# Kernel tuning notes

Hardware: AMD Instinct MI355X
Metric: run time of the kernel (lower is better)

Reference implementation:

```python
import jax, jax.numpy as jnp
import numpy as np

N = 100000
E = 1600000
F_IN = 256
HEADS = 8
C1 = 8
NCLS = 16
NEG_SLOPE = 0.2


def setup_inputs() -> dict:
    key = jax.random.key(0)
    ks = jax.random.split(key, 8)
    x = jax.random.normal(ks[0], (N, F_IN), dtype=jnp.float32)
    edge_index = jax.random.randint(ks[1], (2, E), 0, N, dtype=jnp.int64)
    W1 = jax.random.normal(ks[2], (F_IN, HEADS * C1), dtype=jnp.float32) * (1.0 / np.sqrt(F_IN))
    a1_src = jax.random.normal(ks[3], (HEADS, C1), dtype=jnp.float32) * 0.1
    a1_dst = jax.random.normal(ks[4], (HEADS, C1), dtype=jnp.float32) * 0.1
    b1 = jnp.zeros((HEADS * C1,), dtype=jnp.float32)
    W2 = jax.random.normal(ks[5], (HEADS * C1, NCLS), dtype=jnp.float32) * (1.0 / np.sqrt(HEADS * C1))
    a2_src = jax.random.normal(ks[6], (1, NCLS), dtype=jnp.float32) * 0.1
    a2_dst = jax.random.normal(ks[7], (1, NCLS), dtype=jnp.float32) * 0.1
    b2 = jnp.zeros((NCLS,), dtype=jnp.float32)
    return {"x": x, "edge_index": edge_index, "W1": W1, "a1_src": a1_src,
            "a1_dst": a1_dst, "b1": b1, "W2": W2, "a2_src": a2_src,
            "a2_dst": a2_dst, "b2": b2}


def gat_layer(x, src, dst, W, a_src, a_dst, b, heads, out_c, concat):
    n = x.shape[0]
    h = (x @ W).reshape(n, heads, out_c)            # [N,H,C]
    al_src = (h * a_src).sum(-1)                    # [N,H]
    al_dst = (h * a_dst).sum(-1)                    # [N,H]
    e = jax.nn.leaky_relu(al_src[src] + al_dst[dst], NEG_SLOPE)  # [E',H]
    m = jax.ops.segment_max(e, dst, num_segments=n)              # per-dst max
    alpha = jnp.exp(e - m[dst])
    denom = jax.ops.segment_sum(alpha, dst, num_segments=n)
    alpha = alpha / denom[dst]
    out = jax.ops.segment_sum(h[src] * alpha[:, :, None], dst, num_segments=n)  # [N,H,C]
    out = out.reshape(n, heads * out_c) if concat else out.mean(axis=1)
    return out + b


def reference(x, edge_index, W1, a1_src, a1_dst, b1, W2, a2_src, a2_dst, b2):
    # add self-loops (PyG GATConv default)
    loop = jnp.arange(N, dtype=edge_index.dtype)
    src = jnp.concatenate([edge_index[0], loop])
    dst = jnp.concatenate([edge_index[1], loop])
    # dropout layers are identity in eval mode
    h = jax.nn.elu(gat_layer(x, src, dst, W1, a1_src, a1_dst, b1, HEADS, C1, True))
    out = gat_layer(h, src, dst, W2, a2_src, a2_dst, b2, 1, NCLS, False)
    return jax.nn.log_softmax(out, axis=-1)
```

## Files before the change

kernel.cpp:

```cpp
#include <hip/hip_runtime.h>
#include <math.h>

#define NN   100000
#define EE   1600000
#define FIN  256
#define NCLS 16
#define NEG  0.2f

#define NEDGE (EE + NN)
#define WBKT  256
#define NBKT  ((NN + WBKT - 1) / WBKT)
#define CAP   5120
#define ABLK  4096
#define NABLK ((NEDGE + ABLK - 1) / ABLK)

#define OFF_GCNT  0
#define OFF_BASE  392
#define OFF_ROW   784
#define OFF_BKT   100788
#define OFF_ADJ   (OFF_BKT + NBKT*CAP)
#define OFF_H1B   (OFF_ADJ + NEDGE)
#define OFF_H1E   (OFF_H1B + NN*32)
#define OFF_AL1S  (OFF_H1E + NN*32)
#define OFF_AL1D  (OFF_AL1S + NN*8)
#define OFF_H2B   (OFF_AL1D + NN*8)
#define OFF_AL2S  (OFF_H2B + NN*8)
#define OFF_AL2D  (OFF_AL2S + NN)

__device__ __forceinline__ float lrelu(float x) { return x >= 0.f ? x : NEG * x; }
__device__ __forceinline__ unsigned short f2bf(float x) {
    unsigned u = __float_as_uint(x);
    return (unsigned short)((u + 0x7FFF + ((u >> 16) & 1)) >> 16);
}
__device__ __forceinline__ float bf2f(unsigned short b) {
    return __uint_as_float(((unsigned)b) << 16);
}
__device__ __forceinline__ float bflo(unsigned u) { return __uint_as_float(u << 16); }
__device__ __forceinline__ float bfhi(unsigned u) { return __uint_as_float(u & 0xFFFF0000u); }

__global__ __launch_bounds__(256) void k_binA(
    const int* __restrict__ esrc, const int* __restrict__ edst,
    int* __restrict__ gcnt, unsigned* __restrict__ bkt)
{
    __shared__ int lcnt[NBKT];
    __shared__ int lbase[NBKT];
    const int t = threadIdx.x;
    const int e0 = blockIdx.x * ABLK;
    for (int i = t; i < NBKT; i += 256) lcnt[i] = 0;
    __syncthreads();

    unsigned wrd[16];
    unsigned short bb[16], ll[16];
    #pragma unroll
    for (int j = 0; j < 16; ++j) {
        int ei = e0 + j * 256 + t;
        bb[j] = 0xFFFFu;
        if (ei < NEDGE) {
            int s, d;
            if (ei < EE) { s = esrc[ei]; d = edst[ei]; } else { s = d = ei - EE; }
            int b = d >> 8;
            wrd[j] = ((unsigned)s << 8) | (unsigned)(d & 255);
            bb[j] = (unsigned short)b;
            ll[j] = (unsigned short)atomicAdd(&lcnt[b], 1);
        }
    }
    __syncthreads();
    for (int i = t; i < NBKT; i += 256)
        lbase[i] = lcnt[i] ? atomicAdd(&gcnt[i], lcnt[i]) : 0;
    __syncthreads();
    #pragma unroll
    for (int j = 0; j < 16; ++j) {
        if (bb[j] != 0xFFFFu) {
            int b = bb[j];
            bkt[(size_t)b * CAP + lbase[b] + ll[j]] = wrd[j];
        }
    }
}

__global__ __launch_bounds__(512) void k_scanB(
    const int* __restrict__ gcnt, int* __restrict__ base, int* __restrict__ row)
{
    __shared__ int s[512];
    int t = threadIdx.x;
    int v = (t < NBKT) ? gcnt[t] : 0;
    s[t] = v;
    __syncthreads();
    for (int off = 1; off < 512; off <<= 1) {
        int u = (t >= off) ? s[t - off] : 0;
        __syncthreads();
        s[t] += u;
        __syncthreads();
    }
    if (t <= NBKT) base[t] = s[t] - v;
    if (t == 0) row[NN] = NEDGE;
}

__global__ __launch_bounds__(256) void k_binC(
    const int* __restrict__ gcnt, const int* __restrict__ base,
    const unsigned* __restrict__ bkt, int* __restrict__ row, int* __restrict__ adj)
{
    __shared__ unsigned wd[CAP];
    __shared__ int hist[256], pref[256], cnt2[256];
    const int g = blockIdx.x, t = threadIdx.x;
    const int cn = gcnt[g], bs = base[g];
    hist[t] = 0; cnt2[t] = 0;
    __syncthreads();
    for (int i = t; i < cn; i += 256) {
        unsigned w = bkt[(size_t)g * CAP + i];
        wd[i] = w;
        atomicAdd(&hist[w & 255], 1);
    }
    __syncthreads();
    int v = hist[t];
    pref[t] = v;
    __syncthreads();
    for (int off = 1; off < 256; off <<= 1) {
        int u = (t >= off) ? pref[t - off] : 0;
        __syncthreads();
        pref[t] += u;
        __syncthreads();
    }
    int ex = pref[t] - v;
    int n = g * 256 + t;
    if (n < NN) row[n] = bs + ex;
    pref[t] = ex;
    __syncthreads();
    for (int i = t; i < cn; i += 256) {
        unsigned w = wd[i];
        int dl = w & 255;
        int p = atomicAdd(&cnt2[dl], 1);
        adj[bs + pref[dl] + p] = (int)(w >> 8);
    }
}

__global__ __launch_bounds__(256) void k_gemm1(
    const float* __restrict__ x, const float* __restrict__ W1,
    const float* __restrict__ a1s, const float* __restrict__ a1d,
    unsigned short* __restrict__ h1b, float* __restrict__ al1s, float* __restrict__ al1d)
{
    __shared__ float sxT[32][68];
    __shared__ float sW[32][64];
    const int t = threadIdx.x;
    const int n0 = blockIdx.x * 64;
    const int tr = t >> 4, tc = t & 15;

    float acc[4][4] = {};

    for (int kc = 0; kc < 256; kc += 32) {
        __syncthreads();
        #pragma unroll
        for (int it = 0; it < 2; ++it) {
            int i = t + it * 256;
            int r = i >> 3, fj = i & 7;
            int n = n0 + r;
            float4 v = (n < NN) ? *(const float4*)(x + (size_t)n * FIN + kc + fj * 4)
                                : make_float4(0.f, 0.f, 0.f, 0.f);
            sxT[fj * 4 + 0][r] = v.x;
            sxT[fj * 4 + 1][r] = v.y;
            sxT[fj * 4 + 2][r] = v.z;
            sxT[fj * 4 + 3][r] = v.w;
        }
        #pragma unroll
        for (int it = 0; it < 2; ++it) {
            int i = t + it * 256;
            int r = i >> 4, fj = i & 15;
            *(float4*)&sW[r][fj * 4] = *(const float4*)(W1 + (size_t)(kc + r) * 64 + fj * 4);
        }
        __syncthreads();
        #pragma unroll
        for (int k = 0; k < 32; ++k) {
            float4 a = *(const float4*)&sxT[k][tr * 4];
            float4 b = *(const float4*)&sW[k][tc * 4];
            acc[0][0] += a.x * b.x; acc[0][1] += a.x * b.y; acc[0][2] += a.x * b.z; acc[0][3] += a.x * b.w;
            acc[1][0] += a.y * b.x; acc[1][1] += a.y * b.y; acc[1][2] += a.y * b.z; acc[1][3] += a.y * b.w;
            acc[2][0] += a.z * b.x; acc[2][1] += a.z * b.y; acc[2][2] += a.z * b.z; acc[2][3] += a.z * b.w;
            acc[3][0] += a.w * b.x; acc[3][1] += a.w * b.y; acc[3][2] += a.w * b.z; acc[3][3] += a.w * b.w;
        }
    }

    #pragma unroll
    for (int j = 0; j < 4; ++j) {
        int n = n0 + tr * 4 + j;
        if (n < NN) {
            ushort4 v = make_ushort4(f2bf(acc[j][0]), f2bf(acc[j][1]), f2bf(acc[j][2]), f2bf(acc[j][3]));
            *(ushort4*)(h1b + (size_t)n * 64 + tc * 4) = v;
        }
    }

    float sa[4], da[4];
    #pragma unroll
    for (int u = 0; u < 4; ++u) { sa[u] = a1s[tc * 4 + u]; da[u] = a1d[tc * 4 + u]; }
    #pragma unroll
    for (int j = 0; j < 4; ++j) {
        float vs = acc[j][0] * sa[0] + acc[j][1] * sa[1] + acc[j][2] * sa[2] + acc[j][3] * sa[3];
        float vd = acc[j][0] * da[0] + acc[j][1] * da[1] + acc[j][2] * da[2] + acc[j][3] * da[3];
        vs += __shfl_xor(vs, 1, 64);
        vd += __shfl_xor(vd, 1, 64);
        int n = n0 + tr * 4 + j;
        if (!(tc & 1) && n < NN) {
            al1s[n * 8 + (tc >> 1)] = vs;
            al1d[n * 8 + (tc >> 1)] = vd;
        }
    }
}

__global__ __launch_bounds__(256) void k_agg1(
    const int* __restrict__ row, const int* __restrict__ adj,
    const float* __restrict__ al1s, const float* __restrict__ al1d,
    const unsigned* __restrict__ h1b2, const float* __restrict__ b1,
    unsigned* __restrict__ h1e2)
{
    const int wv = threadIdx.x >> 6, lane = threadIdx.x & 63;
    const int n = blockIdx.x * 4 + wv;
    const int q = lane >> 4;
    const int r = lane & 15;
    const int h = r >> 1;
    const float ald = al1d[n * 8 + h];
    const int r0 = row[n], r1 = row[n + 1];

    float dsum = 0.f, ax = 0.f, ay = 0.f, bx = 0.f, by = 0.f;
    for (int c0 = r0; c0 < r1; c0 += 64) {
        int li = c0 + lane;
        int adjv = adj[li < r1 ? li : r0];
        int m = r1 - c0; if (m > 64) m = 64;
        int k = 0;
        for (; k + 16 <= m; k += 16) {
            int s0 = __shfl(adjv, k + 0  + q, 64);
            int s1 = __shfl(adjv, k + 4  + q, 64);
            int s2 = __shfl(adjv, k + 8  + q, 64);
            int s3 = __shfl(adjv, k + 12 + q, 64);
            float a0 = al1s[s0 * 8 + h];
            float a1 = al1s[s1 * 8 + h];
            float a2 = al1s[s2 * 8 + h];
            float a3 = al1s[s3 * 8 + h];
            uint2 u0 = *(const uint2*)(h1b2 + s0 * 32 + r * 2);
            uint2 u1 = *(const uint2*)(h1b2 + s1 * 32 + r * 2);
            uint2 u2 = *(const uint2*)(h1b2 + s2 * 32 + r * 2);
            uint2 u3 = *(const uint2*)(h1b2 + s3 * 32 + r * 2);
            float w0 = __expf(lrelu(a0 + ald));
            float w1 = __expf(lrelu(a1 + ald));
            float w2 = __expf(lrelu(a2 + ald));
            float w3 = __expf(lrelu(a3 + ald));
            dsum += (w0 + w1) + (w2 + w3);
            ax += w0 * bflo(u0.x) + w1 * bflo(u1.x) + w2 * bflo(u2.x) + w3 * bflo(u3.x);
            ay += w0 * bfhi(u0.x) + w1 * bfhi(u1.x) + w2 * bfhi(u2.x) + w3 * bfhi(u3.x);
            bx += w0 * bflo(u0.y) + w1 * bflo(u1.y) + w2 * bflo(u2.y) + w3 * bflo(u3.y);
            by += w0 * bfhi(u0.y) + w1 * bfhi(u1.y) + w2 * bfhi(u2.y) + w3 * bfhi(u3.y);
        }
        for (; k < m; k += 4) {
            int kk = k + q;
            bool act = kk < m;
            int s0 = __shfl(adjv, act ? kk : 0, 64);
            float w0 = act ? __expf(lrelu(al1s[s0 * 8 + h] + ald)) : 0.f;
            uint2 u0 = *(const uint2*)(h1b2 + s0 * 32 + r * 2);
            dsum += w0;
            ax += w0 * bflo(u0.x);
            ay += w0 * bfhi(u0.x);
            bx += w0 * bflo(u0.y);
            by += w0 * bfhi(u0.y);
        }
    }
    dsum += __shfl_xor(dsum, 16, 64); dsum += __shfl_xor(dsum, 32, 64);
    ax   += __shfl_xor(ax,   16, 64); ax   += __shfl_xor(ax,   32, 64);
    ay   += __shfl_xor(ay,   16, 64); ay   += __shfl_xor(ay,   32, 64);
    bx   += __shfl_xor(bx,   16, 64); bx   += __shfl_xor(bx,   32, 64);
    by   += __shfl_xor(by,   16, 64); by   += __shfl_xor(by,   32, 64);

    float inv = 1.f / dsum;
    float v0 = ax * inv + b1[r * 4 + 0];
    float v1 = ay * inv + b1[r * 4 + 1];
    float v2 = bx * inv + b1[r * 4 + 2];
    float v3 = by * inv + b1[r * 4 + 3];
    v0 = v0 > 0.f ? v0 : __expf(v0) - 1.f;
    v1 = v1 > 0.f ? v1 : __expf(v1) - 1.f;
    v2 = v2 > 0.f ? v2 : __expf(v2) - 1.f;
    v3 = v3 > 0.f ? v3 : __expf(v3) - 1.f;
    if (q == 0) {
        uint2 o;
        o.x = (unsigned)f2bf(v0) | ((unsigned)f2bf(v1) << 16);
        o.y = (unsigned)f2bf(v2) | ((unsigned)f2bf(v3) << 16);
        *(uint2*)(h1e2 + n * 32 + r * 2) = o;
    }
}

__global__ __launch_bounds__(256) void k_gemm2(
    const unsigned short* __restrict__ h1e, const float* __restrict__ W2,
    const float* __restrict__ a2s, const float* __restrict__ a2d,
    unsigned short* __restrict__ h2b, float* __restrict__ al2s, float* __restrict__ al2d)
{
    __shared__ float sW[64 * 16];
    const int t = threadIdx.x;
    for (int i = t; i < 64 * 16; i += 256) sW[i] = W2[i];
    __syncthreads();
    const int n = blockIdx.x * 16 + (t >> 4);
    const int k = t & 15;
    if (n >= NN) return;
    const unsigned short* hr = h1e + (size_t)n * 64;
    float acc = 0.f;
    #pragma unroll
    for (int c = 0; c < 64; ++c) acc += bf2f(hr[c]) * sW[c * 16 + k];
    h2b[(size_t)n * 16 + k] = f2bf(acc);
    float vs = acc * a2s[k], vd = acc * a2d[k];
    #pragma unroll
    for (int off = 1; off < 16; off <<= 1) {
        vs += __shfl_xor(vs, off, 64);
        vd += __shfl_xor(vd, off, 64);
    }
    if (k == 0) { al2s[n] = vs; al2d[n] = vd; }
}

__global__ __launch_bounds__(256) void k_agg2(
    const int* __restrict__ row, const int* __restrict__ adj,
    const float* __restrict__ al2s, const float* __restrict__ al2d,
    const unsigned* __restrict__ h2b2, const float* __restrict__ b2,
    float* __restrict__ out)
{
    const int wv = threadIdx.x >> 6, lane = threadIdx.x & 63;
    const int n = blockIdx.x * 4 + wv;
    const float ald = al2d[n];
    const int r0 = row[n], r1 = row[n + 1];

    const int j = lane >> 2;
    const int r = lane & 3;
    float dsum = 0.f, ax = 0.f, ay = 0.f, bx = 0.f, by = 0.f;
    for (int i = r0; i < r1; i += 16) {
        int i0 = i + j;
        bool act = i0 < r1;
        int s = adj[act ? i0 : r0];
        float w = act ? __expf(lrelu(al2s[s] + ald)) : 0.f;
        uint2 u = *(const uint2*)(h2b2 + s * 8 + r * 2);
        dsum += w;
        ax += w * bflo(u.x);
        ay += w * bfhi(u.x);
        bx += w * bflo(u.y);
        by += w * bfhi(u.y);
    }
    #pragma unroll
    for (int off = 4; off < 64; off <<= 1) {
        dsum += __shfl_xor(dsum, off, 64);
        ax   += __shfl_xor(ax,   off, 64);
        ay   += __shfl_xor(ay,   off, 64);
        bx   += __shfl_xor(bx,   off, 64);
        by   += __shfl_xor(by,   off, 64);
    }
    float inv = 1.f / dsum;
    float v0 = ax * inv + b2[r * 4 + 0];
    float v1 = ay * inv + b2[r * 4 + 1];
    float v2 = bx * inv + b2[r * 4 + 2];
    float v3 = by * inv + b2[r * 4 + 3];

    float mx = fmaxf(fmaxf(v0, v1), fmaxf(v2, v3));
    mx = fmaxf(mx, __shfl_xor(mx, 1, 64));
    mx = fmaxf(mx, __shfl_xor(mx, 2, 64));
    float se = __expf(v0 - mx) + __expf(v1 - mx) + __expf(v2 - mx) + __expf(v3 - mx);
    se += __shfl_xor(se, 1, 64);
    se += __shfl_xor(se, 2, 64);
    float ls = mx + __logf(se);
    if (j == 0)
        *(float4*)(out + (size_t)n * 16 + r * 4) = make_float4(v0 - ls, v1 - ls, v2 - ls, v3 - ls);
}

extern "C" void kernel_launch(void* const* d_in, const int* in_sizes, int n_in,
                              void* d_out, int out_size, void* d_ws, size_t ws_size,
                              hipStream_t stream)
{
    const float* x    = (const float*)d_in[0];
    const int*   eidx = (const int*)d_in[1];
    const float* W1   = (const float*)d_in[2];
    const float* a1s  = (const float*)d_in[3];
    const float* a1d  = (const float*)d_in[4];
    const float* b1   = (const float*)d_in[5];
    const float* W2   = (const float*)d_in[6];
    const float* a2s  = (const float*)d_in[7];
    const float* a2d  = (const float*)d_in[8];
    const float* b2   = (const float*)d_in[9];
    float* out = (float*)d_out;
    float* ws  = (float*)d_ws;

    const int* esrc = eidx;
    const int* edst = eidx + EE;

    int* gcnt = (int*)(ws + OFF_GCNT);
    int* base = (int*)(ws + OFF_BASE);
    int* row  = (int*)(ws + OFF_ROW);
    unsigned* bkt = (unsigned*)(ws + OFF_BKT);
    int* adj  = (int*)(ws + OFF_ADJ);
    unsigned short* h1b = (unsigned short*)(ws + OFF_H1B);
    unsigned short* h1e = (unsigned short*)(ws + OFF_H1E);
    float* al1s  = ws + OFF_AL1S;
    float* al1d  = ws + OFF_AL1D;
    unsigned short* h2b = (unsigned short*)(ws + OFF_H2B);
    float* al2s  = ws + OFF_AL2S;
    float* al2d  = ws + OFF_AL2D;

    hipMemsetAsync(gcnt, 0, 392 * sizeof(int), stream);

    k_binA <<<NABLK, 256, 0, stream>>>(esrc, edst, gcnt, bkt);
    k_scanB<<<1,     512, 0, stream>>>(gcnt, base, row);
    k_binC <<<NBKT,  256, 0, stream>>>(gcnt, base, bkt, row, adj);

    k_gemm1<<<(NN + 63) / 64, 256, 0, stream>>>(x, W1, a1s, a1d, h1b, al1s, al1d);
    k_agg1 <<<NN / 4, 256, 0, stream>>>(row, adj, al1s, al1d, (const unsigned*)h1b, b1, (unsigned*)h1e);
    k_gemm2<<<NN / 16, 256, 0, stream>>>(h1e, W2, a2s, a2d, h2b, al2s, al2d);
    k_agg2 <<<NN / 4, 256, 0, stream>>>(row, adj, al2s, al2d, (const unsigned*)h2b, b2, out);
}
```

Measured before the change: 376.3 us.

## Partition layer-1 aggregation by source range and combine partial softmax sums

Sorts each destination's neighbor list by source partition (four ranges of 25k nodes) during CSR build and records per-partition row offsets. Layer-1 aggregation is split into four partition passes, each gathering only from a quarter of the h1 and al1s tables for better cache locality. Each pass writes fp16 partial weighted averages and denominators, and a combine kernel merges them with bias and ELU. This adds extra partial-buffer traffic, one more kernel launch, serial per-thread sorting work in binC, and fp16 precision loss. The path runs only when the workspace is large enough.

```diff
diff --git a/kernel.cpp b/kernel.cpp
--- a/kernel.cpp
+++ b/kernel.cpp
@@ -1,4 +1,5 @@
 #include <hip/hip_runtime.h>
+#include <hip/hip_fp16.h>
 #include <math.h>
 
 #define NN   100000
@@ -13,6 +14,9 @@
 #define CAP   5120
 #define ABLK  4096
 #define NABLK ((NEDGE + ABLK - 1) / ABLK)
+
+#define NPART 4
+#define PSIZE 25000
 
 #define OFF_GCNT  0
 #define OFF_BASE  392
@@ -26,6 +30,10 @@
 #define OFF_H2B   (OFF_AL1D + NN*8)
 #define OFF_AL2S  (OFF_H2B + NN*8)
 #define OFF_AL2D  (OFF_AL2S + NN)
+#define OFF_ROW2  (OFF_AL2D + NN)
+#define OFF_PVH   (OFF_ROW2 + NN*5 + 8)
+#define OFF_END   (OFF_PVH + NN*128)
+#define OFF_PWH   OFF_BKT
 
 __device__ __forceinline__ float lrelu(float x) { return x >= 0.f ? x : NEG * x; }
 __device__ __forceinline__ unsigned short f2bf(float x) {
@@ -37,6 +45,14 @@
 }
 __device__ __forceinline__ float bflo(unsigned u) { return __uint_as_float(u << 16); }
 __device__ __forceinline__ float bfhi(unsigned u) { return __uint_as_float(u & 0xFFFF0000u); }
+__device__ __forceinline__ unsigned pack2h(float a, float b) {
+    __half2 hh = __floats2half2_rn(a, b);
+    return *reinterpret_cast<unsigned*>(&hh);
+}
+__device__ __forceinline__ float2 unpack2h(unsigned u) {
+    __half2 hh = *reinterpret_cast<__half2*>(&u);
+    return __half22float2(hh);
+}
 
 __global__ __launch_bounds__(256) void k_binA(
     const int* __restrict__ esrc, const int* __restrict__ edst,
@@ -97,13 +113,17 @@
 
 __global__ __launch_bounds__(256) void k_binC(
     const int* __restrict__ gcnt, const int* __restrict__ base,
-    const unsigned* __restrict__ bkt, int* __restrict__ row, int* __restrict__ adj)
+    const unsigned* __restrict__ bkt, int* __restrict__ row, int* __restrict__ adj,
+    int* __restrict__ row2, int wr2)
 {
     __shared__ unsigned wd[CAP];
+    __shared__ unsigned srt[CAP];
     __shared__ int hist[256], pref[256], cnt2[256];
+    __shared__ int h4[256][5];
     const int g = blockIdx.x, t = threadIdx.x;
     const int cn = gcnt[g], bs = base[g];
     hist[t] = 0; cnt2[t] = 0;
+    h4[t][0] = 0; h4[t][1] = 0; h4[t][2] = 0; h4[t][3] = 0;
     __syncthreads();
     for (int i = t; i < cn; i += 256) {
         unsigned w = bkt[(size_t)g * CAP + i];
@@ -129,7 +149,25 @@
         unsigned w = wd[i];
         int dl = w & 255;
         int p = atomicAdd(&cnt2[dl], 1);
-        adj[bs + pref[dl] + p] = (int)(w >> 8);
+        srt[pref[dl] + p] = w >> 8;
+    }
+    __syncthreads();
+    for (int k = 0; k < v; ++k) {
+        unsigned s = srt[ex + k];
+        ++h4[t][s / (unsigned)PSIZE];
+    }
+    int run = 0;
+    #pragma unroll
+    for (int b = 0; b < NPART; ++b) {
+        int c = h4[t][b];
+        if (wr2 && n < NN) row2[n * 5 + b] = bs + ex + run;
+        h4[t][b] = ex + run;
+        run += c;
+    }
+    if (wr2 && n < NN) row2[n * 5 + 4] = bs + ex + v;
+    for (int k = 0; k < v; ++k) {
+        unsigned s = srt[ex + k];
+        adj[bs + h4[t][s / (unsigned)PSIZE]++] = (int)s;
     }
 }
 
@@ -204,6 +242,88 @@
     }
 }
 
+__global__ __launch_bounds__(256) void k_agg1p(
+    const int* __restrict__ row2, const int* __restrict__ adj,
+    const float* __restrict__ al1s, const float* __restrict__ al1d,
+    const unsigned* __restrict__ h1b2,
+    unsigned* __restrict__ pvh, unsigned* __restrict__ pwh)
+{
+    const int p  = blockIdx.x & 3;
+    const int dq = blockIdx.x >> 2;
+    const int wv = threadIdx.x >> 6, lane = threadIdx.x & 63;
+    const int gslot = lane >> 4;
+    const int r  = lane & 15;
+    const int h  = r >> 1;
+    const int n  = dq * 16 + wv * 4 + gslot;
+    const int e0 = row2[n * 5 + p];
+    const int e1 = row2[n * 5 + p + 1];
+    const float ald = al1d[n * 8 + h];
+
+    float dsum = 0.f, ax = 0.f, ay = 0.f, bx = 0.f, by = 0.f;
+    for (int k = e0; k < e1; k += 2) {
+        bool k1ok = (k + 1 < e1);
+        int s0 = __builtin_nontemporal_load(adj + k);
+        int s1 = __builtin_nontemporal_load(adj + (k1ok ? k + 1 : k));
+        float a0 = al1s[s0 * 8 + h];
+        float a1 = al1s[s1 * 8 + h];
+        uint2 u0 = *(const uint2*)(h1b2 + s0 * 32 + r * 2);
+        uint2 u1 = *(const uint2*)(h1b2 + s1 * 32 + r * 2);
+        float w0 = __expf(lrelu(a0 + ald));
+        float w1 = k1ok ? __expf(lrelu(a1 + ald)) : 0.f;
+        dsum += w0 + w1;
+        ax += w0 * bflo(u0.x) + w1 * bflo(u1.x);
+        ay += w0 * bfhi(u0.x) + w1 * bfhi(u1.x);
+        bx += w0 * bflo(u0.y) + w1 * bflo(u1.y);
+        by += w0 * bfhi(u0.y) + w1 * bfhi(u1.y);
+    }
+    float invp = dsum > 0.f ? 1.f / dsum : 0.f;
+    unsigned o0 = pack2h(ax * invp, ay * invp);
+    unsigned o1 = pack2h(bx * invp, by * invp);
+    size_t pb = (size_t)(p * NN + n) * 32 + r * 2;
+    __builtin_nontemporal_store(o0, pvh + pb);
+    __builtin_nontemporal_store(o1, pvh + pb + 1);
+    float dnx = __shfl_xor(dsum, 2, 64);
+    if ((r & 3) == 0)
+        __builtin_nontemporal_store(pack2h(dsum, dnx),
+                                    pwh + (size_t)(p * NN + n) * 4 + (r >> 2));
+}
+
+__global__ __launch_bounds__(256) void k_comb1(
+    const unsigned* __restrict__ pvh, const unsigned* __restrict__ pwh,
+    const float* __restrict__ b1, unsigned* __restrict__ h1e2)
+{
+    const int t = threadIdx.x;
+    const int n = blockIdx.x * 16 + (t >> 4);
+    const int r = t & 15;
+    const int hsel = (r >> 1) & 1;
+    float a0 = 0.f, a1 = 0.f, a2 = 0.f, a3 = 0.f, ds = 0.f;
+    #pragma unroll
+    for (int p = 0; p < NPART; ++p) {
+        size_t pb = (size_t)(p * NN + n) * 32 + r * 2;
+        unsigned u0 = __builtin_nontemporal_load(pvh + pb);
+        unsigned u1 = __builtin_nontemporal_load(pvh + pb + 1);
+        float2 dq = unpack2h(pwh[(size_t)(p * NN + n) * 4 + (r >> 2)]);
+        float dp = hsel ? dq.y : dq.x;
+        float2 f0 = unpack2h(u0), f1 = unpack2h(u1);
+        a0 += dp * f0.x; a1 += dp * f0.y;
+        a2 += dp * f1.x; a3 += dp * f1.y;
+        ds += dp;
+    }
+    float inv = 1.f / ds;
+    float v0 = a0 * inv + b1[r * 4 + 0];
+    float v1 = a1 * inv + b1[r * 4 + 1];
+    float v2 = a2 * inv + b1[r * 4 + 2];
+    float v3 = a3 * inv + b1[r * 4 + 3];
+    v0 = v0 > 0.f ? v0 : __expf(v0) - 1.f;
+    v1 = v1 > 0.f ? v1 : __expf(v1) - 1.f;
+    v2 = v2 > 0.f ? v2 : __expf(v2) - 1.f;
+    v3 = v3 > 0.f ? v3 : __expf(v3) - 1.f;
+    uint2 o;
+    o.x = (unsigned)f2bf(v0) | ((unsigned)f2bf(v1) << 16);
+    o.y = (unsigned)f2bf(v2) | ((unsigned)f2bf(v3) << 16);
+    *(uint2*)(h1e2 + n * 32 + r * 2) = o;
+}
+
 __global__ __launch_bounds__(256) void k_agg1(
     const int* __restrict__ row, const int* __restrict__ adj,
     const float* __restrict__ al1s, const float* __restrict__ al1d,
@@ -219,46 +339,17 @@
     const int r0 = row[n], r1 = row[n + 1];
 
     float dsum = 0.f, ax = 0.f, ay = 0.f, bx = 0.f, by = 0.f;
-    for (int c0 = r0; c0 < r1; c0 += 64) {
-        int li = c0 + lane;
-        int adjv = adj[li < r1 ? li : r0];
-        int m = r1 - c0; if (m > 64) m = 64;
-        int k = 0;
-        for (; k + 16 <= m; k += 16) {
-            int s0 = __shfl(adjv, k + 0  + q, 64);
-            int s1 = __shfl(adjv, k + 4  + q, 64);
-            int s2 = __shfl(adjv, k + 8  + q, 64);
-            int s3 = __shfl(adjv, k + 12 + q, 64);
-            float a0 = al1s[s0 * 8 + h];
-            float a1 = al1s[s1 * 8 + h];
-            float a2 = al1s[s2 * 8 + h];
-            float a3 = al1s[s3 * 8 + h];
-            uint2 u0 = *(const uint2*)(h1b2 + s0 * 32 + r * 2);
-            uint2 u1 = *(const uint2*)(h1b2 + s1 * 32 + r * 2);
-            uint2 u2 = *(const uint2*)(h1b2 + s2 * 32 + r * 2);
-            uint2 u3 = *(const uint2*)(h1b2 + s3 * 32 + r * 2);
-            float w0 = __expf(lrelu(a0 + ald));
-            float w1 = __expf(lrelu(a1 + ald));
-            float w2 = __expf(lrelu(a2 + ald));
-            float w3 = __expf(lrelu(a3 + ald));
-            dsum += (w0 + w1) + (w2 + w3);
-            ax += w0 * bflo(u0.x) + w1 * bflo(u1.x) + w2 * bflo(u2.x) + w3 * bflo(u3.x);
-            ay += w0 * bfhi(u0.x) + w1 * bfhi(u1.x) + w2 * bfhi(u2.x) + w3 * bfhi(u3.x);
-            bx += w0 * bflo(u0.y) + w1 * bflo(u1.y) + w2 * bflo(u2.y) + w3 * bflo(u3.y);
-            by += w0 * bfhi(u0.y) + w1 * bfhi(u1.y) + w2 * bfhi(u2.y) + w3 * bfhi(u3.y);
-        }
-        for (; k < m; k += 4) {
-            int kk = k + q;
-            bool act = kk < m;
-            int s0 = __shfl(adjv, act ? kk : 0, 64);
-            float w0 = act ? __expf(lrelu(al1s[s0 * 8 + h] + ald)) : 0.f;
-            uint2 u0 = *(const uint2*)(h1b2 + s0 * 32 + r * 2);
-            dsum += w0;
-            ax += w0 * bflo(u0.x);
-            ay += w0 * bfhi(u0.x);
-            bx += w0 * bflo(u0.y);
-            by += w0 * bfhi(u0.y);
-        }
+    for (int i = r0; i < r1; i += 4) {
+        int i0 = i + q;
+        bool act = i0 < r1;
+        int s0 = adj[act ? i0 : r0];
+        float w0 = act ? __expf(lrelu(al1s[s0 * 8 + h] + ald)) : 0.f;
+        uint2 u0 = *(const uint2*)(h1b2 + s0 * 32 + r * 2);
+        dsum += w0;
+        ax += w0 * bflo(u0.x);
+        ay += w0 * bfhi(u0.x);
+        bx += w0 * bflo(u0.y);
+        by += w0 * bfhi(u0.y);
     }
     dsum += __shfl_xor(dsum, 16, 64); dsum += __shfl_xor(dsum, 32, 64);
     ax   += __shfl_xor(ax,   16, 64); ax   += __shfl_xor(ax,   32, 64);
@@ -392,15 +483,26 @@
     unsigned short* h2b = (unsigned short*)(ws + OFF_H2B);
     float* al2s  = ws + OFF_AL2S;
     float* al2d  = ws + OFF_AL2D;
+    int* row2 = (int*)(ws + OFF_ROW2);
+    unsigned* pvh = (unsigned*)(ws + OFF_PVH);
+    unsigned* pwh = (unsigned*)(ws + OFF_PWH);
+
+    const bool wide = ws_size >= (size_t)OFF_END * 4;
 
     hipMemsetAsync(gcnt, 0, 392 * sizeof(int), stream);
 
     k_binA <<<NABLK, 256, 0, stream>>>(esrc, edst, gcnt, bkt);
     k_scanB<<<1,     512, 0, stream>>>(gcnt, base, row);
-    k_binC <<<NBKT,  256, 0, stream>>>(gcnt, base, bkt, row, adj);
+    k_binC <<<NBKT,  256, 0, stream>>>(gcnt, base, bkt, row, adj, row2, wide ? 1 : 0);
 
     k_gemm1<<<(NN + 63) / 64, 256, 0, stream>>>(x, W1, a1s, a1d, h1b, al1s, al1d);
-    k_agg1 <<<NN / 4, 256, 0, stream>>>(row, adj, al1s, al1d, (const unsigned*)h1b, b1, (unsigned*)h1e);
+    if (wide) {
+        k_agg1p<<<(NN / 16) * NPART, 256, 0, stream>>>(row2, adj, al1s, al1d,
+                                                       (const unsigned*)h1b, pvh, pwh);
+        k_comb1<<<NN / 16, 256, 0, stream>>>(pvh, pwh, b1, (unsigned*)h1e);
+    } else {
+        k_agg1<<<NN / 4, 256, 0, stream>>>(row, adj, al1s, al1d, (const unsigned*)h1b, b1, (unsigned*)h1e);
+    }
     k_gemm2<<<NN / 16, 256, 0, stream>>>(h1e, W2, a2s, a2d, h2b, al2s, al2d);
     k_agg2 <<<NN / 4, 256, 0, stream>>>(row, adj, al2s, al2d, (const unsigned*)h2b, b2, out);
 }
```

Result: slower. 423.3 us (+12.5%).

## Slice layer-1 features into column blocks and aggregate each slice per block

Applied to the files above, without the earlier changes.

Stores h1 and the source attention logits in four column slices (16 features, 2 heads each) so each aggregation block reads only a 3.2MB slice of the gathered features. This should improve cache hit rates for the random neighbor gathers. The aggregation kernel is restructured to use 8 lanes per destination node with serial per-lane edge loops and non-temporal adjacency loads. In exchange, each edge list is read four times, and lanes in a wave now diverge on differing node degrees.

```diff
diff --git a/kernel.cpp b/kernel.cpp
--- a/kernel.cpp
+++ b/kernel.cpp
@@ -13,6 +13,8 @@
 #define CAP   5120
 #define ABLK  4096
 #define NABLK ((NEDGE + ABLK - 1) / ABLK)
+
+#define NSLC 4
 
 #define OFF_GCNT  0
 #define OFF_BASE  392
@@ -136,7 +138,7 @@
 __global__ __launch_bounds__(256) void k_gemm1(
     const float* __restrict__ x, const float* __restrict__ W1,
     const float* __restrict__ a1s, const float* __restrict__ a1d,
-    unsigned short* __restrict__ h1b, float* __restrict__ al1s, float* __restrict__ al1d)
+    unsigned* __restrict__ h1bS, float* __restrict__ alS, float* __restrict__ al1d)
 {
     __shared__ float sxT[32][68];
     __shared__ float sW[32][64];
@@ -178,12 +180,15 @@
         }
     }
 
+    const int cb = tc >> 2;
     #pragma unroll
     for (int j = 0; j < 4; ++j) {
         int n = n0 + tr * 4 + j;
         if (n < NN) {
-            ushort4 v = make_ushort4(f2bf(acc[j][0]), f2bf(acc[j][1]), f2bf(acc[j][2]), f2bf(acc[j][3]));
-            *(ushort4*)(h1b + (size_t)n * 64 + tc * 4) = v;
+            uint2 o;
+            o.x = (unsigned)f2bf(acc[j][0]) | ((unsigned)f2bf(acc[j][1]) << 16);
+            o.y = (unsigned)f2bf(acc[j][2]) | ((unsigned)f2bf(acc[j][3]) << 16);
+            *(uint2*)(h1bS + ((size_t)cb * NN + n) * 8 + (tc & 3) * 2) = o;
         }
     }
 
@@ -198,93 +203,70 @@
         vd += __shfl_xor(vd, 1, 64);
         int n = n0 + tr * 4 + j;
         if (!(tc & 1) && n < NN) {
-            al1s[n * 8 + (tc >> 1)] = vs;
-            al1d[n * 8 + (tc >> 1)] = vd;
-        }
-    }
-}
-
-__global__ __launch_bounds__(256) void k_agg1(
+            int hh = tc >> 1;
+            alS[((size_t)(hh >> 1) * NN + n) * 2 + (hh & 1)] = vs;
+            al1d[n * 8 + hh] = vd;
+        }
+    }
+}
+
+__global__ __launch_bounds__(256) void k_agg1c(
     const int* __restrict__ row, const int* __restrict__ adj,
-    const float* __restrict__ al1s, const float* __restrict__ al1d,
-    const unsigned* __restrict__ h1b2, const float* __restrict__ b1,
-    unsigned* __restrict__ h1e2)
-{
+    const float* __restrict__ alS, const float* __restrict__ al1d,
+    const unsigned* __restrict__ h1bS, const float* __restrict__ b1,
+    unsigned* __restrict__ h1eS)
+{
+    const int p  = blockIdx.x & 3;
+    const int dq = blockIdx.x >> 2;
     const int wv = threadIdx.x >> 6, lane = threadIdx.x & 63;
-    const int n = blockIdx.x * 4 + wv;
-    const int q = lane >> 4;
-    const int r = lane & 15;
-    const int h = r >> 1;
-    const float ald = al1d[n * 8 + h];
+    const int g  = lane >> 3;
+    const int c  = lane & 7;
+    const int n  = dq * 32 + wv * 8 + g;
+    const int hsel = c >> 2;
+    const float ald = al1d[n * 8 + p * 2 + hsel];
     const int r0 = row[n], r1 = row[n + 1];
-
-    float dsum = 0.f, ax = 0.f, ay = 0.f, bx = 0.f, by = 0.f;
-    for (int c0 = r0; c0 < r1; c0 += 64) {
-        int li = c0 + lane;
-        int adjv = adj[li < r1 ? li : r0];
-        int m = r1 - c0; if (m > 64) m = 64;
-        int k = 0;
-        for (; k + 16 <= m; k += 16) {
-            int s0 = __shfl(adjv, k + 0  + q, 64);
-            int s1 = __shfl(adjv, k + 4  + q, 64);
-            int s2 = __shfl(adjv, k + 8  + q, 64);
-            int s3 = __shfl(adjv, k + 12 + q, 64);
-            float a0 = al1s[s0 * 8 + h];
-            float a1 = al1s[s1 * 8 + h];
-            float a2 = al1s[s2 * 8 + h];
-            float a3 = al1s[s3 * 8 + h];
-            uint2 u0 = *(const uint2*)(h1b2 + s0 * 32 + r * 2);
-            uint2 u1 = *(const uint2*)(h1b2 + s1 * 32 + r * 2);
-            uint2 u2 = *(const uint2*)(h1b2 + s2 * 32 + r * 2);
-            uint2 u3 = *(const uint2*)(h1b2 + s3 * 32 + r * 2);
-            float w0 = __expf(lrelu(a0 + ald));
-            float w1 = __expf(lrelu(a1 + ald));
-            float w2 = __expf(lrelu(a2 + ald));
-            float w3 = __expf(lrelu(a3 + ald));
-            dsum += (w0 + w1) + (w2 + w3);
-            ax += w0 * bflo(u0.x) + w1 * bflo(u1.x) + w2 * bflo(u2.x) + w3 * bflo(u3.x);
-            ay += w0 * bfhi(u0.x) + w1 * bfhi(u1.x) + w2 * bfhi(u2.x) + w3 * bfhi(u3.x);
-            bx += w0 * bflo(u0.y) + w1 * bflo(u1.y) + w2 * bflo(u2.y) + w3 * bflo(u3.y);
-            by += w0 * bfhi(u0.y) + w1 * bfhi(u1.y) + w2 * bfhi(u2.y) + w3 * bfhi(u3.y);
-        }
-        for (; k < m; k += 4) {
-            int kk = k + q;
-            bool act = kk < m;
-            int s0 = __shfl(adjv, act ? kk : 0, 64);
-            float w0 = act ? __expf(lrelu(al1s[s0 * 8 + h] + ald)) : 0.f;
-            uint2 u0 = *(const uint2*)(h1b2 + s0 * 32 + r * 2);
-            dsum += w0;
-            ax += w0 * bflo(u0.x);
-            ay += w0 * bfhi(u0.x);
-            bx += w0 * bflo(u0.y);
-            by += w0 * bfhi(u0.y);
-        }
-    }
-    dsum += __shfl_xor(dsum, 16, 64); dsum += __shfl_xor(dsum, 32, 64);
-    ax   += __shfl_xor(ax,   16, 64); ax   += __shfl_xor(ax,   32, 64);
-    ay   += __shfl_xor(ay,   16, 64); ay   += __shfl_xor(ay,   32, 64);
-    bx   += __shfl_xor(bx,   16, 64); bx   += __shfl_xor(bx,   32, 64);
-    by   += __shfl_xor(by,   16, 64); by   += __shfl_xor(by,   32, 64);
-
+    const float*    alSp = alS + (size_t)p * NN * 2 + hsel;
+    const unsigned* hp   = h1bS + (size_t)p * NN * 8 + c;
+
+    float dsum = 0.f, ax = 0.f, ay = 0.f;
+    int k = r0;
+    for (; k + 3 < r1; k += 4) {
+        int s0 = __builtin_nontemporal_load(adj + k);
+        int s1 = __builtin_nontemporal_load(adj + k + 1);
+        int s2 = __builtin_nontemporal_load(adj + k + 2);
+        int s3 = __builtin_nontemporal_load(adj + k + 3);
+        float a0 = alSp[s0 * 2], a1 = alSp[s1 * 2];
+        float a2 = alSp[s2 * 2], a3 = alSp[s3 * 2];
+        unsigned u0 = hp[s0 * 8], u1 = hp[s1 * 8];
+        unsigned u2 = hp[s2 * 8], u3 = hp[s3 * 8];
+        float w0 = __expf(lrelu(a0 + ald));
+        float w1 = __expf(lrelu(a1 + ald));
+        float w2 = __expf(lrelu(a2 + ald));
+        float w3 = __expf(lrelu(a3 + ald));
+        dsum += (w0 + w1) + (w2 + w3);
+        ax += w0 * bflo(u0) + w1 * bflo(u1) + w2 * bflo(u2) + w3 * bflo(u3);
+        ay += w0 * bfhi(u0) + w1 * bfhi(u1) + w2 * bfhi(u2) + w3 * bfhi(u3);
+    }
+    for (; k < r1; ++k) {
+        int s0 = __builtin_nontemporal_load(adj + k);
+        float w0 = __expf(lrelu(alSp[s0 * 2] + ald));
+        unsigned u0 = hp[s0 * 8];
+        dsum += w0;
+        ax += w0 * bflo(u0);
+        ay += w0 * bfhi(u0);
+    }
     float inv = 1.f / dsum;
-    float v0 = ax * inv + b1[r * 4 + 0];
-    float v1 = ay * inv + b1[r * 4 + 1];
-    float v2 = bx * inv + b1[r * 4 + 2];
-    float v3 = by * inv + b1[r * 4 + 3];
-    v0 = v0 > 0.f ? v0 : __expf(v0) - 1.f;
-    v1 = v1 > 0.f ? v1 : __expf(v1) - 1.f;
-    v2 = v2 > 0.f ? v2 : __expf(v2) - 1.f;
-    v3 = v3 > 0.f ? v3 : __expf(v3) - 1.f;
-    if (q == 0) {
-        uint2 o;
-        o.x = (unsigned)f2bf(v0) | ((unsigned)f2bf(v1) << 16);
-        o.y = (unsigned)f2bf(v2) | ((unsigned)f2bf(v3) << 16);
-        *(uint2*)(h1e2 + n * 32 + r * 2) = o;
-    }
+    float vx = ax * inv + b1[p * 16 + c * 2];
+    float vy = ay * inv + b1[p * 16 + c * 2 + 1];
+    vx = vx > 0.f ? vx : __expf(vx) - 1.f;
+    vy = vy > 0.f ? vy : __expf(vy) - 1.f;
+    __builtin_nontemporal_store(
+        (unsigned)f2bf(vx) | ((unsigned)f2bf(vy) << 16),
+        h1eS + ((size_t)p * NN + n) * 8 + c);
 }
 
 __global__ __launch_bounds__(256) void k_gemm2(
-    const unsigned short* __restrict__ h1e, const float* __restrict__ W2,
+    const unsigned short* __restrict__ h1eS16, const float* __restrict__ W2,
     const float* __restrict__ a2s, const float* __restrict__ a2d,
     unsigned short* __restrict__ h2b, float* __restrict__ al2s, float* __restrict__ al2d)
 {
@@ -295,10 +277,14 @@
     const int n = blockIdx.x * 16 + (t >> 4);
     const int k = t & 15;
     if (n >= NN) return;
-    const unsigned short* hr = h1e + (size_t)n * 64;
     float acc = 0.f;
     #pragma unroll
-    for (int c = 0; c < 64; ++c) acc += bf2f(hr[c]) * sW[c * 16 + k];
+    for (int cb = 0; cb < 4; ++cb) {
+        const unsigned short* hr = h1eS16 + ((size_t)cb * NN + n) * 16;
+        #pragma unroll
+        for (int c = 0; c < 16; ++c)
+            acc += bf2f(hr[c]) * sW[(cb * 16 + c) * 16 + k];
+    }
     h2b[(size_t)n * 16 + k] = f2bf(acc);
     float vs = acc * a2s[k], vd = acc * a2d[k];
     #pragma unroll
@@ -385,9 +371,9 @@
     int* row  = (int*)(ws + OFF_ROW);
     unsigned* bkt = (unsigned*)(ws + OFF_BKT);
     int* adj  = (int*)(ws + OFF_ADJ);
-    unsigned short* h1b = (unsigned short*)(ws + OFF_H1B);
-    unsigned short* h1e = (unsigned short*)(ws + OFF_H1E);
-    float* al1s  = ws + OFF_AL1S;
+    unsigned* h1bS = (unsigned*)(ws + OFF_H1B);
+    unsigned* h1eS = (unsigned*)(ws + OFF_H1E);
+    float* alS   = ws + OFF_AL1S;
     float* al1d  = ws + OFF_AL1D;
     unsigned short* h2b = (unsigned short*)(ws + OFF_H2B);
     float* al2s  = ws + OFF_AL2S;
@@ -399,8 +385,8 @@
     k_scanB<<<1,     512, 0, stream>>>(gcnt, base, row);
     k_binC <<<NBKT,  256, 0, stream>>>(gcnt, base, bkt, row, adj);
 
-    k_gemm1<<<(NN + 63) / 64, 256, 0, stream>>>(x, W1, a1s, a1d, h1b, al1s, al1d);
-    k_agg1 <<<NN / 4, 256, 0, stream>>>(row, adj, al1s, al1d, (const unsigned*)h1b, b1, (unsigned*)h1e);
-    k_gemm2<<<NN / 16, 256, 0, stream>>>(h1e, W2, a2s, a2d, h2b, al2s, al2d);
+    k_gemm1<<<(NN + 63) / 64, 256, 0, stream>>>(x, W1, a1s, a1d, h1bS, alS, al1d);
+    k_agg1c<<<(NN / 32) * NSLC, 256, 0, stream>>>(row, adj, alS, al1d, h1bS, b1, h1eS);
+    k_gemm2<<<NN / 16, 256, 0, stream>>>((const unsigned short*)h1eS, W2, a2s, a2d, h2b, al2s, al2d);
     k_agg2 <<<NN / 4, 256, 0, stream>>>(row, adj, al2s, al2d, (const unsigned*)h2b, b2, out);
 }
```

Result: slower. 432.3 us (+14.9%).
